# Kernel optimization log

Hardware: AMD Instinct MI355X
Metric: run time of the kernel (lower is better)

Reference implementation:

```python
import jax, jax.numpy as jnp
import numpy as np

C = 256
HEADS = 8
HD = C // HEADS
SCALE = HD ** -0.5


def conv1x1(x, W, b):
    # x: [B,C_in,H,W], W: [C_out,C_in], b: [C_out]
    return jnp.einsum('oc,bchw->bohw', W, x) + b[None, :, None, None]


def setup_inputs() -> dict:
    key = jax.random.key(0)
    ks = jax.random.split(key, 12)
    B, H, Wd = 2, 48, 48
    s = C ** -0.5
    return {
        'x': jax.random.normal(ks[0], (B, C, H, Wd), jnp.float32),
        'uncertainty': jax.random.uniform(ks[1], (B, 1, H, Wd), jnp.float32),
        'Wq': jax.random.normal(ks[2], (C, C), jnp.float32) * s,
        'bq': jnp.zeros((C,), jnp.float32),
        'Wk': jax.random.normal(ks[3], (C, C), jnp.float32) * s,
        'bk': jnp.zeros((C,), jnp.float32),
        'Wv': jax.random.normal(ks[4], (C, C), jnp.float32) * s,
        'bv': jnp.zeros((C,), jnp.float32),
        'Wg': jax.random.normal(ks[5], (C, 1), jnp.float32),
        'bg': jnp.zeros((C,), jnp.float32),
        'Wo': jax.random.normal(ks[6], (C, C), jnp.float32) * s,
        'bo': jnp.zeros((C,), jnp.float32),
    }


def reference(x, uncertainty, Wq, bq, Wk, bk, Wv, bv, Wg, bg, Wo, bo):
    B, _, H, Wd = x.shape
    N = H * Wd
    # uncertainty gate (1x1 conv from 1 channel to C channels)
    uw = conv1x1(uncertainty, Wg, bg)            # [B,C,H,W]
    gated_x = x * (1.0 - uw)
    q = conv1x1(gated_x, Wq, bq).reshape(B, HEADS, HD, N)
    k = conv1x1(gated_x, Wk, bk).reshape(B, HEADS, HD, N)
    v = conv1x1(x, Wv, bv).reshape(B, HEADS, HD, N)
    # scores: [B,h,N,N] (query tokens n, key tokens m)
    scores = jnp.einsum('bhdn,bhdm->bhnm', q, k) * SCALE
    u_flat = uncertainty.reshape(B, 1, 1, N)      # mask over key axis
    scores = scores * (1.0 - u_flat)
    attn = jax.nn.softmax(scores, axis=-1)
    out = jnp.einsum('bhnm,bhdm->bhdn', attn, v)  # [B,h,hd,N]
    out = out.reshape(B, C, H, Wd)
    out = conv1x1(out, Wo, bo)
    return out + x
```

## Files before the change

### kernel.cpp

```cpp
#include <hip/hip_runtime.h>
#include <hip/hip_bf16.h>

typedef float f32x4 __attribute__((ext_vector_type(4)));
typedef __bf16 bf16x8 __attribute__((ext_vector_type(8)));
typedef __bf16 bf16x4 __attribute__((ext_vector_type(4)));
typedef short s16x4 __attribute__((ext_vector_type(4)));

constexpr int C = 256;
constexpr int N = 2304;
constexpr int T = 2 * N;

#if __has_builtin(__builtin_amdgcn_exp2f)
#define EXP2F(x) __builtin_amdgcn_exp2f(x)
#else
#define EXP2F(x) exp2f(x)
#endif

__device__ __forceinline__ bf16x8 load_bf8(const __bf16* p) {
    return *reinterpret_cast<const bf16x8*>(p);
}

__device__ __forceinline__ f32x4 mfma32(bf16x8 a, bf16x8 b, f32x4 c) {
    return __builtin_amdgcn_mfma_f32_16x16x32_bf16(a, b, c, 0, 0, 0);
}

#if __has_builtin(__builtin_amdgcn_mfma_f32_16x16x16bf16_1k)
__device__ __forceinline__ f32x4 mfma16(bf16x4 a, bf16x4 b, f32x4 c) {
    return __builtin_amdgcn_mfma_f32_16x16x16bf16_1k(
        __builtin_bit_cast(s16x4, a), __builtin_bit_cast(s16x4, b), c, 0, 0, 0);
}
#else
__device__ __forceinline__ f32x4 mfma16(bf16x4 a, bf16x4 b, f32x4 c) {
    f32x4 d;
    asm volatile("v_mfma_f32_16x16x16_bf16 %0, %1, %2, %3"
                 : "=v"(d) : "v"(a), "v"(b), "v"(c));
    return d;
}
#endif

__device__ __forceinline__ void gload_lds16(const __bf16* g, __bf16* l) {
    __builtin_amdgcn_global_load_lds(
        (const __attribute__((address_space(1))) void*)g,
        (__attribute__((address_space(3))) void*)l, 16, 0, 0);
}

#define VMCNT2() asm volatile("s_waitcnt vmcnt(2)" ::: "memory")
#define VMCNT0() asm volatile("s_waitcnt vmcnt(0)" ::: "memory")
#define LGKM0()  asm volatile("s_waitcnt lgkmcnt(0)" ::: "memory")

__global__ void prep_kernel(const float* __restrict__ x, const float* __restrict__ u,
                            const float* __restrict__ Wg, const float* __restrict__ bg,
                            const float* __restrict__ Wq, const float* __restrict__ Wk,
                            const float* __restrict__ Wv, const float* __restrict__ Wo,
                            __bf16* __restrict__ xT, __bf16* __restrict__ gxT,
                            __bf16* __restrict__ Wb) {
    __shared__ float tile[32][65];
    int t = threadIdx.x;
    if (blockIdx.x >= 576) {
        int u2 = blockIdx.x - 576;
        const float* srcs[4] = {Wq, Wk, Wv, Wo};
        int m = u2 >> 6;
        int idx = (u2 & 63) * 256 + t;
        float4 v = reinterpret_cast<const float4*>(srcs[m])[idx];
        bf16x4 o = { (__bf16)v.x, (__bf16)v.y, (__bf16)v.z, (__bf16)v.w };
        reinterpret_cast<bf16x4*>(Wb + m * 65536)[idx] = o;
        return;
    }
    int uu = blockIdx.x;
    int n0 = (uu % 36) * 64;
    int c0 = ((uu / 36) & 7) * 32;
    int b = uu / 288;
    const float* xp = x + (b * C + c0) * N + n0;
    #pragma unroll
    for (int rr = 0; rr < 8; ++rr) {
        int cl = rr * 4 + (t >> 6);
        int nl = t & 63;
        tile[cl][nl] = xp[cl * N + nl];
    }
    __syncthreads();
    int cq = (t & 7) * 4;
    #pragma unroll
    for (int it = 0; it < 2; ++it) {
        int nl = it * 32 + (t >> 3);
        float uv = u[b * N + n0 + nl];
        bf16x4 xo, go;
        #pragma unroll
        for (int jj = 0; jj < 4; ++jj) {
            int cch = c0 + cq + jj;
            float xv = tile[cq + jj][nl];
            float gate = 1.0f - (Wg[cch] * uv + bg[cch]);
            xo[jj] = (__bf16)xv;
            go[jj] = (__bf16)(xv * gate);
        }
        int tok = b * N + n0 + nl;
        *reinterpret_cast<bf16x4*>(xT + (long)tok * C + c0 + cq) = xo;
        *reinterpret_cast<bf16x4*>(gxT + (long)tok * C + c0 + cq) = go;
    }
}

__global__ __launch_bounds__(256) void qkv_kernel(const __bf16* __restrict__ Wb,
    const __bf16* __restrict__ xT, const __bf16* __restrict__ gxT,
    const float* __restrict__ bq, const float* __restrict__ bk, const float* __restrict__ bv,
    const float* __restrict__ u,
    __bf16* __restrict__ Q, __bf16* __restrict__ K, __bf16* __restrict__ V) {
    int L = blockIdx.x;
    int h = L & 7;
    int rest = L >> 3;
    int c = rest % 36;
    int z = rest / 36;
    int wave = threadIdx.x >> 6, lane = threadIdx.x & 63;
    int g = lane >> 4, r = lane & 15;
    int ow = h * 32 + (wave & 1) * 16;
    int t0 = c * 128 + (wave >> 1) * 64;
    const __bf16* W = Wb + z * 65536;
    const __bf16* inp = (z == 2) ? xT : gxT;
    f32x4 acc[4] = {};
    for (int k = 0; k < 8; ++k) {
        bf16x8 a = load_bf8(W + (ow + r) * C + k * 32 + g * 8);
        #pragma unroll
        for (int tb = 0; tb < 4; ++tb) {
            bf16x8 bfr = load_bf8(inp + (long)(t0 + tb * 16 + r) * C + k * 32 + g * 8);
            acc[tb] = mfma32(a, bfr, acc[tb]);
        }
    }
    const float* bias = (z == 0) ? bq : (z == 1) ? bk : bv;
    float bvw[4];
    #pragma unroll
    for (int i = 0; i < 4; ++i) bvw[i] = bias[ow + g * 4 + i];
    int d0 = (wave & 1) * 16 + g * 4;
    const float SC = 0.17677669529663687f * 1.4426950408889634f;
    #pragma unroll
    for (int tb = 0; tb < 4; ++tb) {
        int t = t0 + tb * 16 + r;
        int b = t / N, n = t % N;
        if (z == 2) {
            #pragma unroll
            for (int i = 0; i < 4; ++i)
                V[((long)(b * 8 + h) * 32 + d0 + i) * N + n] = (__bf16)(acc[tb][i] + bvw[i]);
        } else {
            bf16x4 outv;
            if (z == 1) {
                float scale = SC * (1.0f - u[t]);
                #pragma unroll
                for (int i = 0; i < 4; ++i) outv[i] = (__bf16)((acc[tb][i] + bvw[i]) * scale);
            } else {
                #pragma unroll
                for (int i = 0; i < 4; ++i) outv[i] = (__bf16)(acc[tb][i] + bvw[i]);
            }
            __bf16* dst = (z == 0) ? Q : K;
            *reinterpret_cast<bf16x4*>(dst + ((long)(b * 8 + h) * N + n) * 32 + d0) = outv;
        }
    }
}

__global__ __launch_bounds__(256) void attn_kernel(const __bf16* __restrict__ Q,
    const __bf16* __restrict__ K, const __bf16* __restrict__ V,
    __bf16* __restrict__ aoT) {
    __shared__ __bf16 sK[2][2048];
    __shared__ __bf16 sV[2][2048];
    int id = blockIdx.x;
    int xcd = id & 7, j = id >> 3;
    int bh = xcd + 8 * (j / 36);
    int qblk = j % 36;
    int tid = threadIdx.x;
    int wave = tid >> 6, lane = tid & 63;
    int g = lane >> 4, r = lane & 15;
    int q0w = qblk * 64 + wave * 16;
    const __bf16* Qg = Q + (long)bh * N * 32;
    const __bf16* Kg = K + (long)bh * N * 32;
    const __bf16* Vg = V + (long)bh * 32 * N;
    bf16x8 qf = load_bf8(Qg + (q0w + r) * 32 + g * 8);
    int l_ = tid ^ ((tid >> 3) & 7);
    const __bf16* kS = Kg + (l_ >> 2) * 32 + (l_ & 3) * 8;
    const __bf16* vS = Vg + (long)(l_ >> 3) * N + (l_ & 7) * 8;
    int so = wave * 512;
    auto STAGE = [&](long m0, __bf16* kd, __bf16* vd) {
        gload_lds16(kS + m0 * 32, kd + so);
        gload_lds16(vS + m0,      vd + so);
    };
    int pk[4], pv[4][2];
    #pragma unroll
    for (int t = 0; t < 4; ++t) {
        int ck = (t * 16 + r) * 4 + g;
        pk[t] = (ck ^ ((ck >> 3) & 7)) * 8;
        #pragma unroll
        for (int dt = 0; dt < 2; ++dt) {
            int cv = (dt * 16 + r) * 8 + t * 2 + (g >> 1);
            pv[t][dt] = (cv ^ ((cv >> 3) & 7)) * 8 + (g & 1) * 4;
        }
    }
    bf16x4 onesv;
    #pragma unroll
    for (int i = 0; i < 4; ++i) onesv[i] = (__bf16)1.0f;
    f32x4 oa0 = {}, oa1 = {}, oal = {};
    STAGE(0,  &sK[0][0], &sV[0][0]);
    STAGE(64, &sK[1][0], &sV[1][0]);
    for (int t = 0; t < 36; ++t) {
        if (t < 35) { VMCNT2(); } else { VMCNT0(); }
        __builtin_amdgcn_s_barrier();
        const __bf16* kb = &sK[t & 1][0];
        const __bf16* vb = &sV[t & 1][0];
        bf16x8 kc0 = load_bf8(kb + pk[0]);
        bf16x8 kc1 = load_bf8(kb + pk[1]);
        bf16x8 kc2 = load_bf8(kb + pk[2]);
        bf16x8 kc3 = load_bf8(kb + pk[3]);
        bf16x4 vf[4][2];
        #pragma unroll
        for (int tt = 0; tt < 4; ++tt)
            #pragma unroll
            for (int dt = 0; dt < 2; ++dt)
                vf[tt][dt] = *reinterpret_cast<const bf16x4*>(vb + pv[tt][dt]);
        f32x4 z = {};
        __builtin_amdgcn_s_setprio(1);
        f32x4 s0 = mfma32(kc0, qf, z);
        f32x4 s1 = mfma32(kc1, qf, z);
        f32x4 s2 = mfma32(kc2, qf, z);
        f32x4 s3 = mfma32(kc3, qf, z);
        __builtin_amdgcn_s_setprio(0);
        bf16x4 pa0, pa1, pa2, pa3;
        #pragma unroll
        for (int i = 0; i < 4; ++i) pa0[i] = (__bf16)EXP2F(s0[i]);
        #pragma unroll
        for (int i = 0; i < 4; ++i) pa1[i] = (__bf16)EXP2F(s1[i]);
        #pragma unroll
        for (int i = 0; i < 4; ++i) pa2[i] = (__bf16)EXP2F(s2[i]);
        #pragma unroll
        for (int i = 0; i < 4; ++i) pa3[i] = (__bf16)EXP2F(s3[i]);
        __builtin_amdgcn_s_setprio(1);
        oa0 = mfma16(vf[0][0], pa0, oa0);
        oa1 = mfma16(vf[0][1], pa0, oa1);
        oal = mfma16(onesv,    pa0, oal);
        oa0 = mfma16(vf[1][0], pa1, oa0);
        oa1 = mfma16(vf[1][1], pa1, oa1);
        oal = mfma16(onesv,    pa1, oal);
        oa0 = mfma16(vf[2][0], pa2, oa0);
        oa1 = mfma16(vf[2][1], pa2, oa1);
        oal = mfma16(onesv,    pa2, oal);
        oa0 = mfma16(vf[3][0], pa3, oa0);
        oa1 = mfma16(vf[3][1], pa3, oa1);
        oal = mfma16(onesv,    pa3, oal);
        __builtin_amdgcn_s_setprio(0);
        LGKM0();
        __builtin_amdgcn_s_barrier();
        if (t < 34)
            STAGE((long)(t + 2) * 64, &sK[t & 1][0], &sV[t & 1][0]);
    }
    float inv = 1.0f / oal[0];
    int b = bh >> 3, h = bh & 7;
    long tok = (long)b * N + q0w + r;
    bf16x4 ov0, ov1;
    #pragma unroll
    for (int i = 0; i < 4; ++i) ov0[i] = (__bf16)(oa0[i] * inv);
    #pragma unroll
    for (int i = 0; i < 4; ++i) ov1[i] = (__bf16)(oa1[i] * inv);
    *reinterpret_cast<bf16x4*>(aoT + tok * C + h * 32 + g * 4) = ov0;
    *reinterpret_cast<bf16x4*>(aoT + tok * C + h * 32 + 16 + g * 4) = ov1;
}

__global__ __launch_bounds__(256) void outp_kernel(const __bf16* __restrict__ Wb,
    const __bf16* __restrict__ aoT, const float* __restrict__ bo,
    const float* __restrict__ x, float* __restrict__ out) {
    int o0 = blockIdx.y * 64;
    int t0 = blockIdx.x * 16;
    int wave = threadIdx.x >> 6, lane = threadIdx.x & 63;
    int g = lane >> 4, r = lane & 15;
    int ow = o0 + wave * 16;
    const __bf16* W = Wb + 3 * 65536;
    f32x4 acc = {};
    for (int k = 0; k < 8; ++k) {
        bf16x8 a = load_bf8(W + (ow + r) * C + k * 32 + g * 8);
        bf16x8 bfr = load_bf8(aoT + (long)(t0 + r) * C + k * 32 + g * 8);
        acc = mfma32(a, bfr, acc);
    }
    float bvw[4];
    #pragma unroll
    for (int i = 0; i < 4; ++i) bvw[i] = bo[ow + g * 4 + i];
    int t = t0 + r;
    int b = t / N, n = t % N;
    #pragma unroll
    for (int i = 0; i < 4; ++i) {
        long idx = ((long)b * C + ow + g * 4 + i) * N + n;
        out[idx] = acc[i] + bvw[i] + x[idx];
    }
}

extern "C" void kernel_launch(void* const* d_in, const int* in_sizes, int n_in,
                              void* d_out, int out_size, void* d_ws, size_t ws_size,
                              hipStream_t stream) {
    const float* x  = (const float*)d_in[0];
    const float* u  = (const float*)d_in[1];
    const float* Wq = (const float*)d_in[2];
    const float* bq = (const float*)d_in[3];
    const float* Wk = (const float*)d_in[4];
    const float* bk = (const float*)d_in[5];
    const float* Wv = (const float*)d_in[6];
    const float* bv = (const float*)d_in[7];
    const float* Wg = (const float*)d_in[8];
    const float* bg = (const float*)d_in[9];
    const float* Wo = (const float*)d_in[10];
    const float* bo = (const float*)d_in[11];
    float* out = (float*)d_out;

    char* ws = (char*)d_ws;
    size_t off = 0;
    auto alloc = [&](size_t bytes) {
        char* p = ws + off;
        off += (bytes + 255) & ~(size_t)255;
        return p;
    };
    __bf16* Wb  = (__bf16*)alloc((size_t)4 * 65536 * 2);
    __bf16* xT  = (__bf16*)alloc((size_t)T * C * 2);
    __bf16* gxT = (__bf16*)alloc((size_t)T * C * 2);
    __bf16* Qb  = (__bf16*)alloc((size_t)16 * N * 32 * 2);
    __bf16* Kb  = (__bf16*)alloc((size_t)16 * N * 32 * 2);
    __bf16* Vb  = (__bf16*)alloc((size_t)16 * N * 32 * 2);
    __bf16* aoT = (__bf16*)alloc((size_t)T * C * 2);

    prep_kernel<<<832, 256, 0, stream>>>(x, u, Wg, bg, Wq, Wk, Wv, Wo, xT, gxT, Wb);
    qkv_kernel<<<864, 256, 0, stream>>>(Wb, xT, gxT, bq, bk, bv, u, Qb, Kb, Vb);
    attn_kernel<<<576, 256, 0, stream>>>(Qb, Kb, Vb, aoT);
    outp_kernel<<<dim3(288, 4), 256, 0, stream>>>(Wb, aoT, bo, x, out);
}
```

Before: 76.42 us.

## Split attention key range across two wave groups with LDS reduction

Doubles the attention block to 512 threads and splits the 2304 keys into two halves, each processed by a group of four waves with its own double-buffered LDS staging, so each block runs half as many loop iterations. The partial O accumulators and row sums are then written to shared memory and combined before normalisation and store. This aims to shorten the serial key loop per block and add waves in flight, at the cost of an extra LDS reduction step, two more barriers and larger shared memory per block. Softmax is computed without max subtraction, so the partial sums can be added directly.

```diff
diff --git a/kernel.cpp b/kernel.cpp
--- a/kernel.cpp
+++ b/kernel.cpp
@@ -153,30 +153,33 @@
     }
 }
 
-__global__ __launch_bounds__(256) void attn_kernel(const __bf16* __restrict__ Q,
+__global__ __launch_bounds__(512) void attn_kernel(const __bf16* __restrict__ Q,
     const __bf16* __restrict__ K, const __bf16* __restrict__ V,
     __bf16* __restrict__ aoT) {
-    __shared__ __bf16 sK[2][2048];
-    __shared__ __bf16 sV[2][2048];
+    __shared__ __bf16 sMem[16384];
     int id = blockIdx.x;
     int xcd = id & 7, j = id >> 3;
     int bh = xcd + 8 * (j / 36);
     int qblk = j % 36;
     int tid = threadIdx.x;
     int wave = tid >> 6, lane = tid & 63;
+    int grp = wave >> 2, wv = wave & 3;
     int g = lane >> 4, r = lane & 15;
-    int q0w = qblk * 64 + wave * 16;
+    int q0w = qblk * 64 + wv * 16;
     const __bf16* Qg = Q + (long)bh * N * 32;
-    const __bf16* Kg = K + (long)bh * N * 32;
-    const __bf16* Vg = V + (long)bh * 32 * N;
+    const __bf16* Kg = K + (long)bh * N * 32 + (long)grp * 1152 * 32;
+    const __bf16* Vg = V + (long)bh * 32 * N + grp * 1152;
     bf16x8 qf = load_bf8(Qg + (q0w + r) * 32 + g * 8);
-    int l_ = tid ^ ((tid >> 3) & 7);
+    int s_ = (wv << 6) | lane;
+    int l_ = s_ ^ ((s_ >> 3) & 7);
     const __bf16* kS = Kg + (l_ >> 2) * 32 + (l_ & 3) * 8;
     const __bf16* vS = Vg + (long)(l_ >> 3) * N + (l_ & 7) * 8;
-    int so = wave * 512;
-    auto STAGE = [&](long m0, __bf16* kd, __bf16* vd) {
-        gload_lds16(kS + m0 * 32, kd + so);
-        gload_lds16(vS + m0,      vd + so);
+    __bf16* kB = sMem + grp * 8192;
+    __bf16* vB = kB + 4096;
+    int so = wv * 512;
+    auto STAGE = [&](long m0, int buf) {
+        gload_lds16(kS + m0 * 32, kB + buf * 2048 + so);
+        gload_lds16(vS + m0,      vB + buf * 2048 + so);
     };
     int pk[4], pv[4][2];
     #pragma unroll
@@ -193,13 +196,13 @@
     #pragma unroll
     for (int i = 0; i < 4; ++i) onesv[i] = (__bf16)1.0f;
     f32x4 oa0 = {}, oa1 = {}, oal = {};
-    STAGE(0,  &sK[0][0], &sV[0][0]);
-    STAGE(64, &sK[1][0], &sV[1][0]);
-    for (int t = 0; t < 36; ++t) {
-        if (t < 35) { VMCNT2(); } else { VMCNT0(); }
+    STAGE(0, 0);
+    STAGE(64, 1);
+    for (int t = 0; t < 18; ++t) {
+        if (t < 17) { VMCNT2(); } else { VMCNT0(); }
         __builtin_amdgcn_s_barrier();
-        const __bf16* kb = &sK[t & 1][0];
-        const __bf16* vb = &sV[t & 1][0];
+        const __bf16* kb = kB + (t & 1) * 2048;
+        const __bf16* vb = vB + (t & 1) * 2048;
         bf16x8 kc0 = load_bf8(kb + pk[0]);
         bf16x8 kc1 = load_bf8(kb + pk[1]);
         bf16x8 kc2 = load_bf8(kb + pk[2]);
@@ -242,19 +245,34 @@
         __builtin_amdgcn_s_setprio(0);
         LGKM0();
         __builtin_amdgcn_s_barrier();
-        if (t < 34)
-            STAGE((long)(t + 2) * 64, &sK[t & 1][0], &sV[t & 1][0]);
-    }
-    float inv = 1.0f / oal[0];
-    int b = bh >> 3, h = bh & 7;
-    long tok = (long)b * N + q0w + r;
-    bf16x4 ov0, ov1;
-    #pragma unroll
-    for (int i = 0; i < 4; ++i) ov0[i] = (__bf16)(oa0[i] * inv);
-    #pragma unroll
-    for (int i = 0; i < 4; ++i) ov1[i] = (__bf16)(oa1[i] * inv);
-    *reinterpret_cast<bf16x4*>(aoT + tok * C + h * 32 + g * 4) = ov0;
-    *reinterpret_cast<bf16x4*>(aoT + tok * C + h * 32 + 16 + g * 4) = ov1;
+        if (t < 16)
+            STAGE((long)(t + 2) * 64, t & 1);
+    }
+    __syncthreads();
+    float* F = reinterpret_cast<float*>(sMem);
+    float* D = F + 4096;
+    int fb = (grp * 4 + wv) * 512 + r * 32;
+    int sg = g ^ (r & 7);
+    *reinterpret_cast<f32x4*>(F + fb + sg * 4) = oa0;
+    *reinterpret_cast<f32x4*>(F + fb + (sg ^ 4) * 4) = oa1;
+    if (g == 0) D[grp * 64 + wv * 16 + r] = oal[0];
+    __syncthreads();
+    {
+        int q = tid >> 3;
+        int dg = tid & 7;
+        int qw = q >> 4, qq = q & 15;
+        int off = qw * 512 + qq * 32 + ((dg ^ (qq & 7)) * 4);
+        f32x4 sum = *reinterpret_cast<const f32x4*>(F + off) +
+                    *reinterpret_cast<const f32x4*>(F + 2048 + off);
+        float l = D[qw * 16 + qq] + D[64 + qw * 16 + qq];
+        float inv = 1.0f / l;
+        bf16x4 ov;
+        #pragma unroll
+        for (int i = 0; i < 4; ++i) ov[i] = (__bf16)(sum[i] * inv);
+        int b = bh >> 3, h = bh & 7;
+        *reinterpret_cast<bf16x4*>(
+            aoT + (long)(b * N + qblk * 64 + q) * C + h * 32 + dg * 4) = ov;
+    }
 }
 
 __global__ __launch_bounds__(256) void outp_kernel(const __bf16* __restrict__ Wb,
@@ -318,6 +336,6 @@
 
     prep_kernel<<<832, 256, 0, stream>>>(x, u, Wg, bg, Wq, Wk, Wv, Wo, xT, gxT, Wb);
     qkv_kernel<<<864, 256, 0, stream>>>(Wb, xT, gxT, bq, bk, bv, u, Qb, Kb, Vb);
-    attn_kernel<<<576, 256, 0, stream>>>(Qb, Kb, Vb, aoT);
+    attn_kernel<<<576, 512, 0, stream>>>(Qb, Kb, Vb, aoT);
     outp_kernel<<<dim3(288, 4), 256, 0, stream>>>(Wb, aoT, bo, x, out);
 }
```

New measurement: 68.57 us. 1.11x faster.
